# Optimization experiments

Measured on AMD Instinct MI355X. Metric: run time of the kernel, lower is better.

The kernel has to match this reference:

```python
import jax, jax.numpy as jnp
import numpy as np

DT = 0.02
TMAX = 3.0
NUM_T = 151  # arange(0, Tmax+dt, dt) -> indices 0..150, 150*dt == Tmax == nonspike
THRESH = 1.0
TIMELINE = jnp.arange(NUM_T, dtype=jnp.float32) * DT          # [T]
TIMELINE_REV = jnp.flip(TIMELINE) + 0.1                        # [T]


def linear_spike_fwd(ti, W):
    """ti: [B, Fin] spike times; W: [Fout, Fin] -> out: [B, Fout] spike times."""
    # ramp: relu(t - ti)  -> [B, Fin, T]
    tmp = jax.nn.relu(TIMELINE[None, None, :] - ti[:, :, None])
    # membrane voltage: mem[b,j,t] = sum_i W[j,i] * tmp[b,i,t]  -> [B, Fout, T]
    mem = jnp.einsum('bit,ji->bjt', tmp, W)
    binary = (mem >= THRESH).astype(jnp.float32)
    binary = binary.at[:, :, -1].set(1.0)  # force spike at last timestep
    # reversed-timeline weighting makes argmax pick the FIRST spike index
    idx = jnp.argmax(binary * TIMELINE_REV, axis=2)
    return idx.astype(jnp.float32) * DT


def setup_inputs() -> dict:
    key = jax.random.key(0)
    k1, k2, k3 = jax.random.split(key, 3)
    B, F0, F1, F2 = 64, 1876, 1024, 10
    ti = jax.random.uniform(k1, (B, F0), dtype=jnp.float32)  # spike times in [0,1)
    W1 = 0.002 + 0.002 * jax.random.normal(k2, (F1, F0), dtype=jnp.float32)
    W2 = 0.001 + 0.001 * jax.random.normal(k3, (F2, F1), dtype=jnp.float32)
    return {"ti": ti, "W1": W1, "W2": W2}


def reference(ti, W1, W2):
    h1 = linear_spike_fwd(ti, W1)
    h2 = linear_spike_fwd(h1, W2)
    return h2
```

## Files before the change

kernel.cpp:

```cpp
#include <hip/hip_runtime.h>
#include <stdint.h>

namespace {

constexpr int   B_    = 64;
constexpr int   F0_   = 1876;
constexpr int   F1_   = 1024;
constexpr int   F2_   = 10;
constexpr int   NT_   = 151;
constexpr float DT_   = 0.02f;
constexpr int   NB1_  = 51;
constexpr int   NSTR_ = 2688;
constexpr int   NGT_  = 336;
constexpr int   ROWB_ = 4096;
constexpr float SCL_  = 67108864.0f;
constexpr float ISCL_ = 1.0f / 67108864.0f;

constexpr size_t OFF_W1T  = 0;
constexpr size_t OFF_PAIR = 7688192;
constexpr size_t OFF_GB   = OFF_PAIR + 1376256;
constexpr size_t OFF_GNG  = OFF_GB + 86016;
constexpr size_t OFF_IDX1 = OFF_GNG + 256;

__global__ __launch_bounds__(256) void k_prep(const float* __restrict__ W1,
                                              const float* __restrict__ ti,
                                              float* __restrict__ W1T,
                                              uint2* __restrict__ sPair,
                                              uint32_t* __restrict__ gB,
                                              uint32_t* __restrict__ gNG) {
  __shared__ uint32_t smem[13184];
  const int t = threadIdx.x;
  if (blockIdx.x < 480) {
    float (*tile)[65] = (float (*)[65])smem;
    const int bx = blockIdx.x;
    const int i0 = (bx % 30) * 64;
    const int j0 = (bx / 30) * 64;
    const int c = t & 63, r4 = t >> 6;
    for (int jj = r4; jj < 64; jj += 4) {
      int i = i0 + c;
      tile[c][jj] = (i < F0_) ? W1[(size_t)(j0 + jj) * F0_ + i] : 0.0f;
    }
    __syncthreads();
    for (int ii = r4; ii < 64; ii += 4) {
      int i = i0 + ii;
      if (i <= F0_) W1T[(size_t)i * F1_ + j0 + c] = tile[ii][c];
    }
  } else {
    uint32_t (*hist)[NB1_] = (uint32_t (*)[NB1_])smem;
    uint32_t* pstart = smem + 256 * NB1_;
    uint32_t* cnts   = pstart + 52;
    const int b = blockIdx.x - 480;
    for (int k = 0; k < NB1_; ++k) hist[t][k] = 0;
    __syncthreads();

    const float* tib = ti + (size_t)b * F0_;
    const int n0 = t * 8, n1 = (n0 + 8 < F0_) ? n0 + 8 : F0_;
    for (int n = n0; n < n1; ++n) {
      int k = (int)ceilf(tib[n] * 50.0f);
      k = k < 0 ? 0 : (k > 50 ? 50 : k);
      hist[t][k]++;
    }
    __syncthreads();

    if (t < NB1_) {
      uint32_t run = 0;
      for (int c = 0; c < 256; ++c) { uint32_t x = hist[c][t]; hist[c][t] = run; run += x; }
      cnts[t] = run;
    }
    __syncthreads();
    if (t == 0) {
      uint32_t acc = 0;
      pstart[0] = 0;
      for (int k = 0; k < NB1_; ++k) {
        acc += (cnts[k] + 7u) & ~7u;
        pstart[k + 1] = acc;
      }
      gNG[b] = acc >> 3;
    }
    __syncthreads();

    const uint32_t PT = pstart[NB1_];
    uint2*    out = sPair + (size_t)b * NSTR_;
    uint32_t* gb  = gB + (size_t)b * NGT_;
    const uint2 dummy = make_uint2((uint32_t)F0_ * (uint32_t)ROWB_, 0u);

    for (int n = n0; n < n1; ++n) {
      float v = tib[n];
      int k = (int)ceilf(v * 50.0f);
      k = k < 0 ? 0 : (k > 50 ? 50 : k);
      uint32_t pos = pstart[k] + hist[t][k]++;
      out[pos] = make_uint2((uint32_t)n * (uint32_t)ROWB_, __float_as_uint(v));
    }
    if (t < NB1_) {
      uint32_t s0 = pstart[t] + cnts[t], s1 = pstart[t + 1];
      for (uint32_t s = s0; s < s1; ++s) out[s] = dummy;
      for (uint32_t g = pstart[t] >> 3; g < (s1 >> 3); ++g) gb[g] = (uint32_t)t;
    }
    for (uint32_t s = PT + t; s < (uint32_t)NSTR_; s += 256) out[s] = dummy;
    for (uint32_t g = (PT >> 3) + t; g < (uint32_t)NGT_; g += 256) gb[g] = 80u;
  }
}

__global__ __launch_bounds__(512, 6) void k_main1(const uint2* __restrict__ sPair,
                                                  const uint32_t* __restrict__ gB,
                                                  const uint32_t* __restrict__ gNG,
                                                  const float* __restrict__ W1T,
                                                  uint8_t* __restrict__ idx1) {
  __shared__ uint2    pr[NSTR_];
  __shared__ uint32_t gbw[NGT_];
  __shared__ int binAi[NB1_][64];
  __shared__ int binCi[NB1_][64];
  __shared__ int cand[8][64];
  const int blk  = blockIdx.x;
  const int b    = blk >> 4;
  const int jp   = blk & 15;
  const int tid  = threadIdx.x;
  const int lane = tid & 63;
  const int wv   = __builtin_amdgcn_readfirstlane(tid >> 6);

  {
    const uint4* src = (const uint4*)(sPair + (size_t)b * NSTR_);
    uint4* dst = (uint4*)pr;
    for (int s = tid; s < NSTR_ / 2; s += 512) dst[s] = src[s];
    const uint32_t* gsrc = gB + (size_t)b * NGT_;
    for (int s = tid; s < NGT_; s += 512) gbw[s] = gsrc[s];
    int4* p = (int4*)(&binAi[0][0]);
    for (int s = tid; s < (NB1_ * 64 * 2) / 4; s += 512) p[s] = make_int4(0, 0, 0, 0);
  }
  __syncthreads();

  const uint32_t NG = gNG[b];
  const int q  = (int)(NG >> 3), rr = (int)(NG & 7);
  const int g0  = wv * q + (wv < rr ? wv : rr);
  const int cnt = q + (wv < rr ? 1 : 0);

  const char* wb = (const char*)W1T;
  const uint32_t col4 = (uint32_t)((jp << 6) + lane) * 4u;

  float SA = 0.f, SC = 0.f, SAp = 0.f, SCp = 0.f;
  uint32_t kcur;

  uint32_t rA[8], rB[8], hA, hB;
  float    tA[8], tB[8];
  float    WA[8], WB[8];

#define LOADP(S, g) { const int gg = (g) <= (NGT_ - 1) ? (g) : (NGT_ - 1);    \
  _Pragma("unroll") for (int q2 = 0; q2 < 4; ++q2) {                          \
    uint4 x = *(const uint4*)(&pr[gg * 8 + q2 * 2]);                          \
    r##S[2 * q2]     = x.x; t##S[2 * q2]     = __uint_as_float(x.y);          \
    r##S[2 * q2 + 1] = x.z; t##S[2 * q2 + 1] = __uint_as_float(x.w); }        \
  h##S = gbw[gg]; }

#define ISSW(S) { _Pragma("unroll") for (int e = 0; e < 8; ++e)               \
    W##S[e] = *(const float*)(wb + (size_t)(r##S[e] + col4)); }

#define DUMP() { if (kcur < (uint32_t)NB1_) {                                 \
    atomicAdd(&binAi[kcur][lane], __float2int_rn((SA - SAp) * SCL_));         \
    atomicAdd(&binCi[kcur][lane], __float2int_rn((SC - SCp) * SCL_)); }       \
  SAp = SA; SCp = SC; }

#define PROC(S) {                                                             \
  uint32_t kg = __builtin_amdgcn_readfirstlane(h##S);                         \
  if (kg != kcur) { DUMP(); kcur = kg; }                                      \
  _Pragma("unroll") for (int e = 0; e < 8; ++e) {                             \
    SA += W##S[e]; SC = fmaf(W##S[e], t##S[e], SC); } }

#define STEP(Scur, Snxt, g)                                                   \
  LOADP(Snxt, g); ISSW(Snxt);                                                 \
  __builtin_amdgcn_sched_barrier(0);                                          \
  PROC(Scur);

  LOADP(A, g0); ISSW(A);
  __builtin_amdgcn_sched_barrier(0);
  kcur = __builtin_amdgcn_readfirstlane(hA);

  int m = 0;
#pragma unroll 1
  for (; m + 2 <= cnt; m += 2) {
    STEP(A, B, g0 + m + 1);
    STEP(B, A, g0 + m + 2);
  }
  if (m < cnt) { PROC(A); }
  DUMP();

#undef STEP
#undef PROC
#undef DUMP
#undef ISSW
#undef LOADP

  __syncthreads();

  {
    float SA2 = 0.f, SC2 = 0.f;
    int cnd = 151;
    const int t0 = wv * 19;
    const int t1 = (t0 + 19 < NT_) ? t0 + 19 : NT_;
    for (int tt = 0; tt < t1; ++tt) {
      if (tt < NB1_) {
        SA2 += (float)binAi[tt][lane] * ISCL_;
        SC2 += (float)binCi[tt][lane] * ISCL_;
      }
      if (tt >= t0 && cnd == 151) {
        float mv = (float)tt * DT_ * SA2 - SC2;
        if (mv >= 1.0f) cnd = tt;
      }
    }
    cand[wv][lane] = cnd;
  }
  __syncthreads();
  if (tid < 64) {
    int id = cand[0][tid];
#pragma unroll
    for (int w = 1; w < 8; ++w) id = min(id, cand[w][tid]);
    id = min(id, NT_ - 1);
    idx1[((size_t)b << 10) + (jp << 6) + tid] = (uint8_t)id;
  }
}

__global__ __launch_bounds__(256) void k_main2(const uint8_t* __restrict__ idx1,
                                               const float* __restrict__ W2,
                                               float* __restrict__ out) {
  __shared__ float wrow[F1_];
  __shared__ float tirow[F1_];
  __shared__ float part[4][3][64];
  const int blk = blockIdx.x;
  const int b   = blk / 10;
  const int j   = blk - b * 10;
  const int tid = threadIdx.x;
  const int lane = tid & 63, wvv = tid >> 6;

  const float*   w = W2  + (size_t)j * F1_;
  const uint8_t* h = idx1 + (size_t)b * F1_;
  for (int s = tid; s < F1_; s += 256) {
    wrow[s]  = w[s];
    tirow[s] = (float)h[s] * DT_;
  }
  __syncthreads();

  const float tl0 = (float)lane * DT_;
  const float tl1 = (float)(lane + 64) * DT_;
  const float tl2 = (float)(lane + 128) * DT_;
  float m0 = 0.f, m1 = 0.f, m2 = 0.f;
  const int i0 = wvv * 256;
#pragma unroll 4
  for (int i = i0; i < i0 + 256; ++i) {
    float tiv = tirow[i], ww = wrow[i];
    m0 = fmaf(ww, fmaxf(tl0 - tiv, 0.f), m0);
    m1 = fmaf(ww, fmaxf(tl1 - tiv, 0.f), m1);
    m2 = fmaf(ww, fmaxf(tl2 - tiv, 0.f), m2);
  }
  part[wvv][0][lane] = m0;
  part[wvv][1][lane] = m1;
  part[wvv][2][lane] = m2;
  __syncthreads();

  if (wvv == 0) {
    m0 = part[0][0][lane] + part[1][0][lane] + part[2][0][lane] + part[3][0][lane];
    m1 = part[0][1][lane] + part[1][1][lane] + part[2][1][lane] + part[3][1][lane];
    m2 = part[0][2][lane] + part[1][2][lane] + part[2][2][lane] + part[3][2][lane];
    unsigned long long b0 = __ballot(m0 >= 1.0f);
    unsigned long long b1 = __ballot(m1 >= 1.0f);
    unsigned long long b2 = __ballot(m2 >= 1.0f);
    b2 &= (1ull << 23) - 1;
    b2 |= (1ull << 22);
    int tres;
    if (b0)      tres = __ffsll((long long)b0) - 1;
    else if (b1) tres = 64 + __ffsll((long long)b1) - 1;
    else         tres = 128 + __ffsll((long long)b2) - 1;
    if (lane == 0) out[(size_t)b * F2_ + j] = (float)tres * DT_;
  }
}

}

extern "C" void kernel_launch(void* const* d_in, const int* in_sizes, int n_in,
                              void* d_out, int out_size, void* d_ws, size_t ws_size,
                              hipStream_t stream) {
  const float* ti = (const float*)d_in[0];
  const float* W1 = (const float*)d_in[1];
  const float* W2 = (const float*)d_in[2];
  float* out = (float*)d_out;

  char* ws = (char*)d_ws;
  float*    W1T  = (float*)(ws + OFF_W1T);
  uint2*    sPr  = (uint2*)(ws + OFF_PAIR);
  uint32_t* gBp  = (uint32_t*)(ws + OFF_GB);
  uint32_t* gNGp = (uint32_t*)(ws + OFF_GNG);
  uint8_t*  idx1 = (uint8_t*)(ws + OFF_IDX1);

  hipLaunchKernelGGL(k_prep,  dim3(544),  dim3(256), 0, stream, W1, ti, W1T, sPr, gBp, gNGp);
  hipLaunchKernelGGL(k_main1, dim3(1024), dim3(512), 0, stream, sPr, gBp, gNGp, W1T, idx1);
  hipLaunchKernelGGL(k_main2, dim3(640),  dim3(256), 0, stream, idx1, W2, out);
}
```

Baseline: 73.88 us.

## Widen main1 blocks to 128 columns with float2 loads and direct global pair reads

Each k_main1 block now handles 128 output neurons with 1024 threads. Each lane loads a float2 of W1T and keeps two sets of accumulators. The LDS staging of the sorted pair list is removed and the pairs are read straight from global memory. The hand-written double-buffered software prefetch is replaced by a simple loop. The intent is to halve redundant pair and bin traffic per neuron and to widen weight loads. The risks are more exposed load latency without the explicit pipelining, and more LDS atomics per lane.

```diff
diff --git a/kernel.cpp b/kernel.cpp
--- a/kernel.cpp
+++ b/kernel.cpp
@@ -101,120 +101,102 @@
   }
 }
 
-__global__ __launch_bounds__(512, 6) void k_main1(const uint2* __restrict__ sPair,
-                                                  const uint32_t* __restrict__ gB,
-                                                  const uint32_t* __restrict__ gNG,
-                                                  const float* __restrict__ W1T,
-                                                  uint8_t* __restrict__ idx1) {
-  __shared__ uint2    pr[NSTR_];
-  __shared__ uint32_t gbw[NGT_];
-  __shared__ int binAi[NB1_][64];
-  __shared__ int binCi[NB1_][64];
-  __shared__ int cand[8][64];
+__global__ __launch_bounds__(1024, 4) void k_main1(const uint2* __restrict__ sPair,
+                                                   const uint32_t* __restrict__ gB,
+                                                   const uint32_t* __restrict__ gNG,
+                                                   const float* __restrict__ W1T,
+                                                   uint8_t* __restrict__ idx1) {
+  __shared__ int binAi[NB1_][128];
+  __shared__ int binCi[NB1_][128];
+  __shared__ int cand[8][128];
   const int blk  = blockIdx.x;
-  const int b    = blk >> 4;
-  const int jp   = blk & 15;
+  const int b    = blk >> 3;
+  const int jp   = blk & 7;
   const int tid  = threadIdx.x;
   const int lane = tid & 63;
   const int wv   = __builtin_amdgcn_readfirstlane(tid >> 6);
 
   {
-    const uint4* src = (const uint4*)(sPair + (size_t)b * NSTR_);
-    uint4* dst = (uint4*)pr;
-    for (int s = tid; s < NSTR_ / 2; s += 512) dst[s] = src[s];
-    const uint32_t* gsrc = gB + (size_t)b * NGT_;
-    for (int s = tid; s < NGT_; s += 512) gbw[s] = gsrc[s];
     int4* p = (int4*)(&binAi[0][0]);
-    for (int s = tid; s < (NB1_ * 64 * 2) / 4; s += 512) p[s] = make_int4(0, 0, 0, 0);
+    for (int s = tid; s < (NB1_ * 128 * 2) / 4; s += 1024) p[s] = make_int4(0, 0, 0, 0);
   }
   __syncthreads();
 
   const uint32_t NG = gNG[b];
-  const int q  = (int)(NG >> 3), rr = (int)(NG & 7);
+  const int q  = (int)(NG >> 4), rr = (int)(NG & 15);
   const int g0  = wv * q + (wv < rr ? wv : rr);
   const int cnt = q + (wv < rr ? 1 : 0);
 
-  const char* wb = (const char*)W1T;
-  const uint32_t col4 = (uint32_t)((jp << 6) + lane) * 4u;
-
-  float SA = 0.f, SC = 0.f, SAp = 0.f, SCp = 0.f;
-  uint32_t kcur;
-
-  uint32_t rA[8], rB[8], hA, hB;
-  float    tA[8], tB[8];
-  float    WA[8], WB[8];
-
-#define LOADP(S, g) { const int gg = (g) <= (NGT_ - 1) ? (g) : (NGT_ - 1);    \
-  _Pragma("unroll") for (int q2 = 0; q2 < 4; ++q2) {                          \
-    uint4 x = *(const uint4*)(&pr[gg * 8 + q2 * 2]);                          \
-    r##S[2 * q2]     = x.x; t##S[2 * q2]     = __uint_as_float(x.y);          \
-    r##S[2 * q2 + 1] = x.z; t##S[2 * q2 + 1] = __uint_as_float(x.w); }        \
-  h##S = gbw[gg]; }
-
-#define ISSW(S) { _Pragma("unroll") for (int e = 0; e < 8; ++e)               \
-    W##S[e] = *(const float*)(wb + (size_t)(r##S[e] + col4)); }
-
-#define DUMP() { if (kcur < (uint32_t)NB1_) {                                 \
-    atomicAdd(&binAi[kcur][lane], __float2int_rn((SA - SAp) * SCL_));         \
-    atomicAdd(&binCi[kcur][lane], __float2int_rn((SC - SCp) * SCL_)); }       \
-  SAp = SA; SCp = SC; }
-
-#define PROC(S) {                                                             \
-  uint32_t kg = __builtin_amdgcn_readfirstlane(h##S);                         \
-  if (kg != kcur) { DUMP(); kcur = kg; }                                      \
-  _Pragma("unroll") for (int e = 0; e < 8; ++e) {                             \
-    SA += W##S[e]; SC = fmaf(W##S[e], t##S[e], SC); } }
-
-#define STEP(Scur, Snxt, g)                                                   \
-  LOADP(Snxt, g); ISSW(Snxt);                                                 \
-  __builtin_amdgcn_sched_barrier(0);                                          \
-  PROC(Scur);
-
-  LOADP(A, g0); ISSW(A);
-  __builtin_amdgcn_sched_barrier(0);
-  kcur = __builtin_amdgcn_readfirstlane(hA);
-
-  int m = 0;
+  const uint2*    __restrict__ prb = sPair + (size_t)b * NSTR_;
+  const uint32_t* __restrict__ gb  = gB + (size_t)b * NGT_;
+  const char* wbl = (const char*)W1T + (size_t)((jp << 9) + (lane << 3));
+
+  float SA0 = 0.f, SC0 = 0.f, SA1 = 0.f, SC1 = 0.f;
+  float SA0p = 0.f, SC0p = 0.f, SA1p = 0.f, SC1p = 0.f;
+  uint32_t kcur = 0xFFFFFFFFu;
+
+  auto dump = [&]() {
+    if (kcur < (uint32_t)NB1_) {
+      atomicAdd(&binAi[kcur][2 * lane],     __float2int_rn((SA0 - SA0p) * SCL_));
+      atomicAdd(&binCi[kcur][2 * lane],     __float2int_rn((SC0 - SC0p) * SCL_));
+      atomicAdd(&binAi[kcur][2 * lane + 1], __float2int_rn((SA1 - SA1p) * SCL_));
+      atomicAdd(&binCi[kcur][2 * lane + 1], __float2int_rn((SC1 - SC1p) * SCL_));
+    }
+    SA0p = SA0; SC0p = SC0; SA1p = SA1; SC1p = SC1;
+  };
+
+#define ELEM(rv, tv) {                                                        \
+    float2 w = *(const float2*)(wbl + (rv));                                  \
+    float tiv = __uint_as_float(tv);                                          \
+    SA0 += w.x; SC0 = fmaf(w.x, tiv, SC0);                                    \
+    SA1 += w.y; SC1 = fmaf(w.y, tiv, SC1); }
+
 #pragma unroll 1
-  for (; m + 2 <= cnt; m += 2) {
-    STEP(A, B, g0 + m + 1);
-    STEP(B, A, g0 + m + 2);
-  }
-  if (m < cnt) { PROC(A); }
-  DUMP();
-
-#undef STEP
-#undef PROC
-#undef DUMP
-#undef ISSW
-#undef LOADP
+  for (int m = 0; m < cnt; ++m) {
+    const int g = g0 + m;
+    uint32_t kg = gb[g];
+    uint4 q0 = *(const uint4*)(prb + g * 8 + 0);
+    uint4 q1 = *(const uint4*)(prb + g * 8 + 2);
+    uint4 q2 = *(const uint4*)(prb + g * 8 + 4);
+    uint4 q3 = *(const uint4*)(prb + g * 8 + 6);
+    kg = __builtin_amdgcn_readfirstlane(kg);
+    if (kg != kcur) { dump(); kcur = kg; }
+    ELEM(q0.x, q0.y); ELEM(q0.z, q0.w);
+    ELEM(q1.x, q1.y); ELEM(q1.z, q1.w);
+    ELEM(q2.x, q2.y); ELEM(q2.z, q2.w);
+    ELEM(q3.x, q3.y); ELEM(q3.z, q3.w);
+  }
+  dump();
+#undef ELEM
 
   __syncthreads();
 
   {
+    const int jh = wv & 1, tq = wv >> 1;
+    const int col = jh * 64 + lane;
     float SA2 = 0.f, SC2 = 0.f;
     int cnd = 151;
-    const int t0 = wv * 19;
+    const int t0 = tq * 19;
     const int t1 = (t0 + 19 < NT_) ? t0 + 19 : NT_;
     for (int tt = 0; tt < t1; ++tt) {
       if (tt < NB1_) {
-        SA2 += (float)binAi[tt][lane] * ISCL_;
-        SC2 += (float)binCi[tt][lane] * ISCL_;
+        SA2 += (float)binAi[tt][col] * ISCL_;
+        SC2 += (float)binCi[tt][col] * ISCL_;
       }
       if (tt >= t0 && cnd == 151) {
         float mv = (float)tt * DT_ * SA2 - SC2;
         if (mv >= 1.0f) cnd = tt;
       }
     }
-    cand[wv][lane] = cnd;
-  }
-  __syncthreads();
-  if (tid < 64) {
+    cand[tq][col] = cnd;
+  }
+  __syncthreads();
+  if (tid < 128) {
     int id = cand[0][tid];
 #pragma unroll
     for (int w = 1; w < 8; ++w) id = min(id, cand[w][tid]);
     id = min(id, NT_ - 1);
-    idx1[((size_t)b << 10) + (jp << 6) + tid] = (uint8_t)id;
+    idx1[((size_t)b << 10) + (jp << 7) + tid] = (uint8_t)id;
   }
 }
 
@@ -289,7 +271,7 @@
   uint32_t* gNGp = (uint32_t*)(ws + OFF_GNG);
   uint8_t*  idx1 = (uint8_t*)(ws + OFF_IDX1);
 
-  hipLaunchKernelGGL(k_prep,  dim3(544),  dim3(256), 0, stream, W1, ti, W1T, sPr, gBp, gNGp);
-  hipLaunchKernelGGL(k_main1, dim3(1024), dim3(512), 0, stream, sPr, gBp, gNGp, W1T, idx1);
-  hipLaunchKernelGGL(k_main2, dim3(640),  dim3(256), 0, stream, idx1, W2, out);
-}
+  hipLaunchKernelGGL(k_prep,  dim3(544), dim3(256),  0, stream, W1, ti, W1T, sPr, gBp, gNGp);
+  hipLaunchKernelGGL(k_main1, dim3(512), dim3(1024), 0, stream, sPr, gBp, gNGp, W1T, idx1);
+  hipLaunchKernelGGL(k_main2, dim3(640), dim3(256),  0, stream, idx1, W2, out);
+}
```

Measured after the change: 75.60 us. 2.3% more time.
